# Performance work log

Hardware: AMD Instinct MI355X
Metric: run time of the kernel (lower is better)

Reference implementation:

```python
import jax, jax.numpy as jnp
import numpy as np

N_NODES = 100000
N_EDGES = 1600000
IN_CH, HID_CH, OUT_CH = 128, 64, 64
NEG_SLOPE = 0.2
EPS = 1e-16


def setup_inputs() -> dict:
    key = jax.random.key(0)
    ks = jax.random.split(key, 10)
    x = jax.random.normal(ks[0], (N_NODES, IN_CH), dtype=jnp.float32)
    edge_index = jax.random.randint(ks[1], (2, N_EDGES), 0, N_NODES, dtype=jnp.int64)
    s1 = 1.0 / np.sqrt(IN_CH)
    s2 = 1.0 / np.sqrt(HID_CH)
    return {
        "x": x,
        "edge_index": edge_index,
        "W1": jax.random.normal(ks[2], (IN_CH, HID_CH), dtype=jnp.float32) * s1,
        "a_src1": jax.random.normal(ks[3], (HID_CH,), dtype=jnp.float32) * s2,
        "a_dst1": jax.random.normal(ks[4], (HID_CH,), dtype=jnp.float32) * s2,
        "b1": jnp.zeros((HID_CH,), dtype=jnp.float32),
        "W2": jax.random.normal(ks[5], (HID_CH, OUT_CH), dtype=jnp.float32) * s2,
        "a_src2": jax.random.normal(ks[6], (OUT_CH,), dtype=jnp.float32) * (1.0 / np.sqrt(OUT_CH)),
        "a_dst2": jax.random.normal(ks[7], (OUT_CH,), dtype=jnp.float32) * (1.0 / np.sqrt(OUT_CH)),
        "b2": jnp.zeros((OUT_CH,), dtype=jnp.float32),
    }


def gat_conv(x, src, dst, W, a_s, a_d, b):
    # node projection: [N, d_out]
    h = x @ W
    # per-node attention halves, gathered per edge
    alpha = jax.nn.leaky_relu((h @ a_s)[src] + (h @ a_d)[dst], NEG_SLOPE)  # [E]
    # segment softmax over edges grouped by destination node
    m = jax.ops.segment_max(alpha, dst, num_segments=N_NODES)
    e = jnp.exp(alpha - m[dst])
    z = jax.ops.segment_sum(e, dst, num_segments=N_NODES)
    w = e / (z[dst] + EPS)  # [E]
    # weighted scatter-sum of source features
    out = jax.ops.segment_sum(h[src] * w[:, None], dst, num_segments=N_NODES)
    return out + b


def reference(x, edge_index, W1, a_src1, a_dst1, b1, W2, a_src2, a_dst2, b2):
    # add self loops once (PyG add_self_loops=True in both convs)
    loops = jnp.arange(N_NODES, dtype=edge_index.dtype)
    src = jnp.concatenate([edge_index[0], loops])
    dst = jnp.concatenate([edge_index[1], loops])
    h = jax.nn.relu(gat_conv(x, src, dst, W1, a_src1, a_dst1, b1))
    return gat_conv(h, src, dst, W2, a_src2, a_dst2, b2)
```

## Files before the change

kernel.cpp:

```cpp
#include <hip/hip_runtime.h>
#include <cstdint>

#define NN 100000
#define NX 8
#define NEG 0.2f

__global__ void k_detect(const void* e, int* mode) {
    if (threadIdx.x == 0 && blockIdx.x == 0) {
        const int* p = (const int*)e;
        int allz = 1;
        for (int i = 0; i < 64; ++i)
            if (p[2 * i + 1] != 0) { allz = 0; break; }
        mode[0] = allz;
    }
}

__global__ void k_zero(int* p, int n) {
    int i = blockIdx.x * 256 + threadIdx.x;
    if (i < n) p[i] = 0;
}

__global__ void k_count(const void* e, long E, const int* mode, int* cnt) {
    long i = (long)blockIdx.x * 256 + threadIdx.x;
    if (i >= E) return;
    const int x = (int)(blockIdx.x & (NX - 1));
    long d;
    if (mode[0]) d = (long)((const long long*)e)[E + i];
    else         d = ((const int*)e)[E + i];
    atomicAdd(&cnt[(long)x * NN + d], 1);
}

__global__ void k_scan_block(const int* cnt, int* S, int* bsums, int n) {
    __shared__ int sm[256];
    int i = blockIdx.x * 256 + threadIdx.x;
    int v = (i < n) ? cnt[i] : 0;
    sm[threadIdx.x] = v;
    __syncthreads();
    for (int off = 1; off < 256; off <<= 1) {
        int t = (threadIdx.x >= off) ? sm[threadIdx.x - off] : 0;
        __syncthreads();
        sm[threadIdx.x] += t;
        __syncthreads();
    }
    if (i < n) S[i] = sm[threadIdx.x] - v;
    if (threadIdx.x == 255) bsums[blockIdx.x] = sm[255];
}

__global__ void k_scan_mid(int* bs, int nb) {
    __shared__ int sm[1024];
    __shared__ int carry_s;
    const int t = threadIdx.x;
    if (t == 0) carry_s = 0;
    __syncthreads();
    for (int r = 0; r * 1024 < nb; ++r) {
        int i = r * 1024 + t;
        int v = (i < nb) ? bs[i] : 0;
        sm[t] = v;
        __syncthreads();
        for (int off = 1; off < 1024; off <<= 1) {
            int tv = (t >= off) ? sm[t - off] : 0;
            __syncthreads();
            sm[t] += tv;
            __syncthreads();
        }
        int carry = carry_s;
        if (i < nb) bs[i] = sm[t] - v + carry;
        __syncthreads();
        if (t == 1023) carry_s = carry + sm[1023];
        __syncthreads();
    }
}

__global__ void k_scan_add(int* S, const int* bsums, int n) {
    int i = blockIdx.x * 256 + threadIdx.x;
    if (i < n) S[i] += bsums[blockIdx.x];
}

__global__ void k_fill(const void* e, long E, const int* mode, int* S, int* csr) {
    long i = (long)blockIdx.x * 256 + threadIdx.x;
    if (i >= E) return;
    const int x = (int)(blockIdx.x & (NX - 1));
    long s, d;
    if (mode[0]) {
        const long long* p = (const long long*)e;
        s = (long)p[i]; d = (long)p[E + i];
    } else {
        const int* p = (const int*)e;
        s = p[i]; d = p[E + i];
    }
    int pos = atomicAdd(&S[(long)x * NN + d], 1);
    csr[pos] = (int)s;
}

__global__ void k_reorder(const int* cnt, const int* Send, const int* csr,
                          int* csr2, int* rowptr2, long E, int n) {
    int d = blockIdx.x * 256 + threadIdx.x;
    if (d >= n) return;
    int C = 0, sum = 0;
    int st[NX], cx[NX];
#pragma unroll
    for (int x = 0; x < NX; ++x) {
        int c0 = cnt[(long)x * NN];
        int e0 = Send[(long)x * NN];
        C += e0 - c0;
        int c = cnt[(long)x * NN + d];
        int en = Send[(long)x * NN + d];
        cx[x] = c;
        st[x] = en - c;
        sum += en - c;
    }
    int start = sum - C;
    rowptr2[d] = start;
    if (d == 0) rowptr2[n] = (int)E;
#pragma unroll
    for (int x = 0; x < NX; ++x) {
        int c = cx[x], s0 = st[x];
        for (int j = 0; j < c; ++j) csr2[start++] = csr[s0 + j];
    }
}

template <int K>
__global__ __launch_bounds__(256) void k_gemm_attn(
    const float* __restrict__ X, const float* __restrict__ W,
    const float* __restrict__ As, const float* __restrict__ Ad,
    float* __restrict__ H, float* __restrict__ AS, float* __restrict__ AD, int n) {
    constexpr int KC = 32;
    __shared__ float Wl[KC * 64];
    __shared__ float Xt[KC][68];
    const int tid = threadIdx.x;
    const int tx = tid & 15, ty = tid >> 4;
    const long row0 = (long)blockIdx.x * 64;
    float acc[4][4] = {{0.f}};

    for (int k0 = 0; k0 < K; k0 += KC) {
        __syncthreads();
        {
            const float4* src = (const float4*)(W + (long)k0 * 64);
            float4* dst = (float4*)Wl;
            for (int i = tid; i < KC * 64 / 4; i += 256) dst[i] = src[i];
        }
        {
            const int rr = tid >> 3;
            const int kq = tid & 7;
#pragma unroll
            for (int h = 0; h < 2; ++h) {
                int r = rr + h * 32;
                long row = row0 + r;
                if (row >= n) row = n - 1;
                float4 v = *(const float4*)(X + row * K + k0 + kq * 4);
                Xt[kq * 4 + 0][r] = v.x;
                Xt[kq * 4 + 1][r] = v.y;
                Xt[kq * 4 + 2][r] = v.z;
                Xt[kq * 4 + 3][r] = v.w;
            }
        }
        __syncthreads();
#pragma unroll
        for (int kk = 0; kk < KC; ++kk) {
            float4 xv = *(const float4*)(&Xt[kk][ty * 4]);
            float4 wv = *(const float4*)(&Wl[kk * 64 + tx * 4]);
            acc[0][0] += xv.x * wv.x; acc[0][1] += xv.x * wv.y;
            acc[0][2] += xv.x * wv.z; acc[0][3] += xv.x * wv.w;
            acc[1][0] += xv.y * wv.x; acc[1][1] += xv.y * wv.y;
            acc[1][2] += xv.y * wv.z; acc[1][3] += xv.y * wv.w;
            acc[2][0] += xv.z * wv.x; acc[2][1] += xv.z * wv.y;
            acc[2][2] += xv.z * wv.z; acc[2][3] += xv.z * wv.w;
            acc[3][0] += xv.w * wv.x; acc[3][1] += xv.w * wv.y;
            acc[3][2] += xv.w * wv.z; acc[3][3] += xv.w * wv.w;
        }
    }

#pragma unroll
    for (int i = 0; i < 4; ++i) {
        long row = row0 + ty * 4 + i;
        if (row < n) {
            float4 o = {acc[i][0], acc[i][1], acc[i][2], acc[i][3]};
            *(float4*)(H + row * 64 + tx * 4) = o;
        }
    }
    float4 asv = *(const float4*)(As + tx * 4);
    float4 adv = *(const float4*)(Ad + tx * 4);
#pragma unroll
    for (int i = 0; i < 4; ++i) {
        float ps = acc[i][0] * asv.x + acc[i][1] * asv.y + acc[i][2] * asv.z + acc[i][3] * asv.w;
        float pd = acc[i][0] * adv.x + acc[i][1] * adv.y + acc[i][2] * adv.z + acc[i][3] * adv.w;
#pragma unroll
        for (int off = 1; off < 16; off <<= 1) {
            ps += __shfl_xor(ps, off);
            pd += __shfl_xor(pd, off);
        }
        if (tx == 0) {
            long row = row0 + ty * 4 + i;
            if (row < n) { AS[row] = ps; AD[row] = pd; }
        }
    }
}

__global__ __launch_bounds__(256) void k_agg(
    const int* __restrict__ rowptr, const int* __restrict__ csr,
    const float* __restrict__ AS, const float* __restrict__ AD,
    const float* __restrict__ H, const float* __restrict__ B,
    float* __restrict__ OUT, int n, int relu) {
    const int lane = threadIdx.x & 63;
    const int node = blockIdx.x * 4 + (threadIdx.x >> 6);
    if (node >= n) return;
    const int beg = rowptr[node], end = rowptr[node + 1];
    const int degI = end - beg;
    const int degT = degI + 1;
    const float ad = AD[node];

    float acc = 0.f;
    if (degT <= 64) {
        const bool v = lane < degT;
        int s = (lane < degI) ? csr[beg + lane] : node;
        float a = v ? AS[s] + ad : -__builtin_inff();
        a = (a >= 0.f) ? a : NEG * a;
        float m = a;
#pragma unroll
        for (int off = 32; off; off >>= 1) m = fmaxf(m, __shfl_xor(m, off));
        float ez = v ? __expf(a - m) : 0.f;
        float z = ez;
#pragma unroll
        for (int off = 32; off; off >>= 1) z += __shfl_xor(z, off);
        float wgt = ez * (1.f / (z + 1e-16f));
        int j = 0;
        for (; j + 8 <= degT; j += 8) {
            int s0 = __shfl(s, j),     s1 = __shfl(s, j + 1);
            int s2 = __shfl(s, j + 2), s3 = __shfl(s, j + 3);
            int s4 = __shfl(s, j + 4), s5 = __shfl(s, j + 5);
            int s6 = __shfl(s, j + 6), s7 = __shfl(s, j + 7);
            float w0 = __shfl(wgt, j),     w1 = __shfl(wgt, j + 1);
            float w2 = __shfl(wgt, j + 2), w3 = __shfl(wgt, j + 3);
            float w4 = __shfl(wgt, j + 4), w5 = __shfl(wgt, j + 5);
            float w6 = __shfl(wgt, j + 6), w7 = __shfl(wgt, j + 7);
            float h0 = H[(long)s0 * 64 + lane];
            float h1 = H[(long)s1 * 64 + lane];
            float h2 = H[(long)s2 * 64 + lane];
            float h3 = H[(long)s3 * 64 + lane];
            float h4 = H[(long)s4 * 64 + lane];
            float h5 = H[(long)s5 * 64 + lane];
            float h6 = H[(long)s6 * 64 + lane];
            float h7 = H[(long)s7 * 64 + lane];
            acc += w0 * h0 + w1 * h1 + w2 * h2 + w3 * h3;
            acc += w4 * h4 + w5 * h5 + w6 * h6 + w7 * h7;
        }
        for (; j < degT; ++j) {
            int sj = __shfl(s, j);
            float wj = __shfl(wgt, j);
            acc += wj * H[(long)sj * 64 + lane];
        }
    } else {
        float m = -__builtin_inff(), z = 0.f;
        for (int p0 = 0; p0 < degT; p0 += 64) {
            int e = p0 + lane;
            bool v = e < degT;
            int s = (e < degI) ? csr[beg + e] : node;
            float a = v ? AS[s] + ad : -__builtin_inff();
            a = (a >= 0.f) ? a : NEG * a;
            float cm = a;
#pragma unroll
            for (int off = 32; off; off >>= 1) cm = fmaxf(cm, __shfl_xor(cm, off));
            float mn = fmaxf(m, cm);
            float ez = v ? __expf(a - mn) : 0.f;
#pragma unroll
            for (int off = 32; off; off >>= 1) ez += __shfl_xor(ez, off);
            z = (p0 == 0) ? ez : z * __expf(m - mn) + ez;
            m = mn;
        }
        const float invz = 1.f / (z + 1e-16f);
        for (int p0 = 0; p0 < degT; p0 += 64) {
            int e = p0 + lane;
            bool v = e < degT;
            int s = (e < degI) ? csr[beg + e] : node;
            float wgt = 0.f;
            if (v) {
                float a = AS[s] + ad;
                a = (a >= 0.f) ? a : NEG * a;
                wgt = __expf(a - m) * invz;
            }
            int cntv = min(64, degT - p0);
            for (int j = 0; j < cntv; ++j) {
                int sj = __shfl(s, j);
                float wj = __shfl(wgt, j);
                acc += wj * H[(long)sj * 64 + lane];
            }
        }
    }
    acc += B[lane];
    if (relu) acc = fmaxf(acc, 0.f);
    OUT[(long)node * 64 + lane] = acc;
}

extern "C" void kernel_launch(void* const* d_in, const int* in_sizes, int n_in,
                              void* d_out, int out_size, void* d_ws, size_t ws_size,
                              hipStream_t stream) {
    const float* x   = (const float*)d_in[0];
    const void*  eix = d_in[1];
    const float* W1  = (const float*)d_in[2];
    const float* as1 = (const float*)d_in[3];
    const float* ad1 = (const float*)d_in[4];
    const float* b1  = (const float*)d_in[5];
    const float* W2  = (const float*)d_in[6];
    const float* as2 = (const float*)d_in[7];
    const float* ad2 = (const float*)d_in[8];
    const float* b2  = (const float*)d_in[9];
    float* out = (float*)d_out;

    const int  n  = NN;
    const long E  = (long)in_sizes[1] / 2;
    const int  NS = NX * NN;

    char* w = (char*)d_ws;
    size_t off = 0;
    auto alloc = [&](size_t bytes) -> void* {
        void* p = w + off;
        off = (off + bytes + 255) & ~(size_t)255;
        return p;
    };
    int*   mode    = (int*)alloc(4);
    int*   cnt     = (int*)alloc((size_t)NS * 4);
    int*   S       = (int*)alloc((size_t)NS * 4);
    int*   bsums   = (int*)alloc(4096 * 4);
    int*   csr     = (int*)alloc((size_t)E * 4);
    int*   csr2    = (int*)alloc((size_t)E * 4);
    int*   rowptr2 = (int*)alloc((size_t)(n + 1) * 4);
    float* H       = (float*)alloc((size_t)n * 64 * 4);
    float* AS      = (float*)alloc((size_t)n * 4);
    float* AD      = (float*)alloc((size_t)n * 4);

    const int nbS = (NS + 255) / 256;
    const int nbE = (int)((E + 255) / 256);
    const int nbN = (n + 255) / 256;
    const int nbG = (n + 63) / 64;

    k_detect<<<1, 64, 0, stream>>>(eix, mode);
    k_zero<<<nbS, 256, 0, stream>>>(cnt, NS);
    k_count<<<nbE, 256, 0, stream>>>(eix, E, mode, cnt);
    k_scan_block<<<nbS, 256, 0, stream>>>(cnt, S, bsums, NS);
    k_scan_mid<<<1, 1024, 0, stream>>>(bsums, nbS);
    k_scan_add<<<nbS, 256, 0, stream>>>(S, bsums, NS);
    k_fill<<<nbE, 256, 0, stream>>>(eix, E, mode, S, csr);
    k_reorder<<<nbN, 256, 0, stream>>>(cnt, S, csr, csr2, rowptr2, E, n);

    k_gemm_attn<128><<<nbG, 256, 0, stream>>>(x, W1, as1, ad1, H, AS, AD, n);
    k_agg<<<(n + 3) / 4, 256, 0, stream>>>(rowptr2, csr2, AS, AD, H, b1, out, n, 1);
    k_gemm_attn<64><<<nbG, 256, 0, stream>>>(out, W2, as2, ad2, H, AS, AD, n);
    k_agg<<<(n + 3) / 4, 256, 0, stream>>>(rowptr2, csr2, AS, AD, H, b2, out, n, 0);
}
```

Measured before the change: 461.2 us.

## Record per-edge atomic rank in count pass to make CSR fill atomic-free

The count pass now saves each edge's atomicAdd return value (its rank within its destination bucket) packed with the destination into a combo array. The fill pass then writes csr at S[bucket]+rank without a second round of atomics, and reorder reads exclusive starts directly from S. The detect and zero kernels are merged, each thread handles two edges, and the scan uses 1024-wide blocks so the mid-level scan fits in one pass. This adds an E-sized combo buffer with extra write and read traffic, and assumes ranks fit in 15 bits.

```diff
diff --git a/kernel.cpp b/kernel.cpp
--- a/kernel.cpp
+++ b/kernel.cpp
@@ -5,94 +5,106 @@
 #define NX 8
 #define NEG 0.2f
 
-__global__ void k_detect(const void* e, int* mode) {
-    if (threadIdx.x == 0 && blockIdx.x == 0) {
-        const int* p = (const int*)e;
-        int allz = 1;
-        for (int i = 0; i < 64; ++i)
-            if (p[2 * i + 1] != 0) { allz = 0; break; }
-        mode[0] = allz;
-    }
-}
-
-__global__ void k_zero(int* p, int n) {
+__global__ void k_zero_detect(int* p, int n, const void* e, int* mode) {
     int i = blockIdx.x * 256 + threadIdx.x;
     if (i < n) p[i] = 0;
-}
-
-__global__ void k_count(const void* e, long E, const int* mode, int* cnt) {
-    long i = (long)blockIdx.x * 256 + threadIdx.x;
-    if (i >= E) return;
+    if (blockIdx.x == 0 && threadIdx.x == 0) {
+        const int* q = (const int*)e;
+        int allz = 1;
+        for (int j = 0; j < 64; ++j)
+            if (q[2 * j + 1] != 0) { allz = 0; break; }
+        mode[0] = allz;
+    }
+}
+
+__global__ void k_count(const void* e, long E, const int* mode, int* cnt,
+                        unsigned* combo) {
+    long i0 = ((long)blockIdx.x * 256 + threadIdx.x) * 2;
+    if (i0 >= E) return;
     const int x = (int)(blockIdx.x & (NX - 1));
-    long d;
-    if (mode[0]) d = (long)((const long long*)e)[E + i];
-    else         d = ((const int*)e)[E + i];
-    atomicAdd(&cnt[(long)x * NN + d], 1);
+    const bool has1 = (i0 + 1) < E;
+    int d0, d1 = 0;
+    if (mode[0]) {
+        const long long* p = (const long long*)e;
+        d0 = (int)p[E + i0];
+        if (has1) d1 = (int)p[E + i0 + 1];
+    } else {
+        const int* p = (const int*)e;
+        d0 = p[E + i0];
+        if (has1) d1 = p[E + i0 + 1];
+    }
+    int r0 = atomicAdd(&cnt[x * NN + d0], 1);
+    combo[i0] = ((unsigned)r0 << 17) | (unsigned)d0;
+    if (has1) {
+        int r1 = atomicAdd(&cnt[x * NN + d1], 1);
+        combo[i0 + 1] = ((unsigned)r1 << 17) | (unsigned)d1;
+    }
 }
 
 __global__ void k_scan_block(const int* cnt, int* S, int* bsums, int n) {
-    __shared__ int sm[256];
-    int i = blockIdx.x * 256 + threadIdx.x;
+    __shared__ int sm[1024];
+    const int t = threadIdx.x;
+    int i = blockIdx.x * 1024 + t;
     int v = (i < n) ? cnt[i] : 0;
-    sm[threadIdx.x] = v;
+    sm[t] = v;
     __syncthreads();
-    for (int off = 1; off < 256; off <<= 1) {
-        int t = (threadIdx.x >= off) ? sm[threadIdx.x - off] : 0;
-        __syncthreads();
-        sm[threadIdx.x] += t;
-        __syncthreads();
-    }
-    if (i < n) S[i] = sm[threadIdx.x] - v;
-    if (threadIdx.x == 255) bsums[blockIdx.x] = sm[255];
+    for (int off = 1; off < 1024; off <<= 1) {
+        int tv = (t >= off) ? sm[t - off] : 0;
+        __syncthreads();
+        sm[t] += tv;
+        __syncthreads();
+    }
+    if (i < n) S[i] = sm[t] - v;
+    if (t == 1023) bsums[blockIdx.x] = sm[1023];
 }
 
 __global__ void k_scan_mid(int* bs, int nb) {
     __shared__ int sm[1024];
-    __shared__ int carry_s;
     const int t = threadIdx.x;
-    if (t == 0) carry_s = 0;
+    int v = (t < nb) ? bs[t] : 0;
+    sm[t] = v;
     __syncthreads();
-    for (int r = 0; r * 1024 < nb; ++r) {
-        int i = r * 1024 + t;
-        int v = (i < nb) ? bs[i] : 0;
-        sm[t] = v;
-        __syncthreads();
-        for (int off = 1; off < 1024; off <<= 1) {
-            int tv = (t >= off) ? sm[t - off] : 0;
-            __syncthreads();
-            sm[t] += tv;
-            __syncthreads();
-        }
-        int carry = carry_s;
-        if (i < nb) bs[i] = sm[t] - v + carry;
-        __syncthreads();
-        if (t == 1023) carry_s = carry + sm[1023];
-        __syncthreads();
-    }
+    for (int off = 1; off < 1024; off <<= 1) {
+        int tv = (t >= off) ? sm[t - off] : 0;
+        __syncthreads();
+        sm[t] += tv;
+        __syncthreads();
+    }
+    if (t < nb) bs[t] = sm[t] - v;
 }
 
 __global__ void k_scan_add(int* S, const int* bsums, int n) {
-    int i = blockIdx.x * 256 + threadIdx.x;
+    int i = blockIdx.x * 1024 + threadIdx.x;
     if (i < n) S[i] += bsums[blockIdx.x];
 }
 
-__global__ void k_fill(const void* e, long E, const int* mode, int* S, int* csr) {
-    long i = (long)blockIdx.x * 256 + threadIdx.x;
-    if (i >= E) return;
+__global__ void k_fill(const void* e, long E, const int* mode, const int* S,
+                       const unsigned* combo, int* csr) {
+    long i0 = ((long)blockIdx.x * 256 + threadIdx.x) * 2;
+    if (i0 >= E) return;
     const int x = (int)(blockIdx.x & (NX - 1));
-    long s, d;
+    const bool has1 = (i0 + 1) < E;
+    long s0, s1 = 0;
     if (mode[0]) {
         const long long* p = (const long long*)e;
-        s = (long)p[i]; d = (long)p[E + i];
+        s0 = p[i0];
+        if (has1) s1 = p[i0 + 1];
     } else {
         const int* p = (const int*)e;
-        s = p[i]; d = p[E + i];
-    }
-    int pos = atomicAdd(&S[(long)x * NN + d], 1);
-    csr[pos] = (int)s;
-}
-
-__global__ void k_reorder(const int* cnt, const int* Send, const int* csr,
+        s0 = p[i0];
+        if (has1) s1 = p[i0 + 1];
+    }
+    unsigned c0 = combo[i0];
+    int d0 = (int)(c0 & 0x1FFFFu), r0 = (int)(c0 >> 17);
+    csr[S[x * NN + d0] + r0] = (int)s0;
+    if (has1) {
+        unsigned c1 = combo[i0 + 1];
+        int d1 = (int)(c1 & 0x1FFFFu), r1 = (int)(c1 >> 17);
+        csr[S[x * NN + d1] + r1] = (int)s1;
+    }
+}
+
+__global__ void k_reorder(const int* cnt, const int* S, const int* csr,
                           int* csr2, int* rowptr2, long E, int n) {
     int d = blockIdx.x * 256 + threadIdx.x;
     if (d >= n) return;
@@ -100,14 +112,10 @@
     int st[NX], cx[NX];
 #pragma unroll
     for (int x = 0; x < NX; ++x) {
-        int c0 = cnt[(long)x * NN];
-        int e0 = Send[(long)x * NN];
-        C += e0 - c0;
-        int c = cnt[(long)x * NN + d];
-        int en = Send[(long)x * NN + d];
-        cx[x] = c;
-        st[x] = en - c;
-        sum += en - c;
+        C += S[(long)x * NN];
+        st[x] = S[(long)x * NN + d];
+        cx[x] = cnt[(long)x * NN + d];
+        sum += st[x];
     }
     int start = sum - C;
     rowptr2[d] = start;
@@ -317,29 +325,30 @@
         off = (off + bytes + 255) & ~(size_t)255;
         return p;
     };
-    int*   mode    = (int*)alloc(4);
-    int*   cnt     = (int*)alloc((size_t)NS * 4);
-    int*   S       = (int*)alloc((size_t)NS * 4);
-    int*   bsums   = (int*)alloc(4096 * 4);
-    int*   csr     = (int*)alloc((size_t)E * 4);
-    int*   csr2    = (int*)alloc((size_t)E * 4);
-    int*   rowptr2 = (int*)alloc((size_t)(n + 1) * 4);
-    float* H       = (float*)alloc((size_t)n * 64 * 4);
-    float* AS      = (float*)alloc((size_t)n * 4);
-    float* AD      = (float*)alloc((size_t)n * 4);
-
-    const int nbS = (NS + 255) / 256;
-    const int nbE = (int)((E + 255) / 256);
-    const int nbN = (n + 255) / 256;
-    const int nbG = (n + 63) / 64;
-
-    k_detect<<<1, 64, 0, stream>>>(eix, mode);
-    k_zero<<<nbS, 256, 0, stream>>>(cnt, NS);
-    k_count<<<nbE, 256, 0, stream>>>(eix, E, mode, cnt);
-    k_scan_block<<<nbS, 256, 0, stream>>>(cnt, S, bsums, NS);
+    int*      mode    = (int*)alloc(4);
+    int*      cnt     = (int*)alloc((size_t)NS * 4);
+    int*      S       = (int*)alloc((size_t)NS * 4);
+    int*      bsums   = (int*)alloc(1024 * 4);
+    unsigned* combo   = (unsigned*)alloc((size_t)E * 4);
+    int*      csr     = (int*)alloc((size_t)E * 4);
+    int*      csr2    = (int*)alloc((size_t)E * 4);
+    int*      rowptr2 = (int*)alloc((size_t)(n + 1) * 4);
+    float*    H       = (float*)alloc((size_t)n * 64 * 4);
+    float*    AS      = (float*)alloc((size_t)n * 4);
+    float*    AD      = (float*)alloc((size_t)n * 4);
+
+    const int nbZ  = (NS + 255) / 256;
+    const int nbE2 = (int)((E + 511) / 512);
+    const int nbS  = (NS + 1023) / 1024;
+    const int nbN  = (n + 255) / 256;
+    const int nbG  = (n + 63) / 64;
+
+    k_zero_detect<<<nbZ, 256, 0, stream>>>(cnt, NS, eix, mode);
+    k_count<<<nbE2, 256, 0, stream>>>(eix, E, mode, cnt, combo);
+    k_scan_block<<<nbS, 1024, 0, stream>>>(cnt, S, bsums, NS);
     k_scan_mid<<<1, 1024, 0, stream>>>(bsums, nbS);
-    k_scan_add<<<nbS, 256, 0, stream>>>(S, bsums, NS);
-    k_fill<<<nbE, 256, 0, stream>>>(eix, E, mode, S, csr);
+    k_scan_add<<<nbS, 1024, 0, stream>>>(S, bsums, NS);
+    k_fill<<<nbE2, 256, 0, stream>>>(eix, E, mode, S, combo, csr);
     k_reorder<<<nbN, 256, 0, stream>>>(cnt, S, csr, csr2, rowptr2, E, n);
 
     k_gemm_attn<128><<<nbG, 256, 0, stream>>>(x, W1, as1, ad1, H, AS, AD, n);
```

Result: faster. 399.3 us (-13.4%).
